# Kernel tuning notes

Measured on AMD Instinct MI355X. Metric: run time of the kernel, lower is better.

## Reference

```python
import jax, jax.numpy as jnp
import numpy as np

B, S, H, NH = 1, 4096, 768, 12
D = H // NH  # per-head dim = 64


def setup_inputs() -> dict:
    key = jax.random.key(0)
    ks = jax.random.split(key, 10)
    p = 0.02  # param scale
    return {
        "x": jax.random.normal(ks[0], (B, S, H), jnp.float32),
        "Wq": jax.random.normal(ks[1], (H, H), jnp.float32) * p,
        "bq": jax.random.normal(ks[2], (H,), jnp.float32) * p,
        "Wk": jax.random.normal(ks[3], (H, H), jnp.float32) * p,
        "bk": jax.random.normal(ks[4], (H,), jnp.float32) * p,
        "Wv": jax.random.normal(ks[5], (H, H), jnp.float32) * p,
        "bv": jax.random.normal(ks[6], (H,), jnp.float32) * p,
        "Wo": jax.random.normal(ks[7], (H, H), jnp.float32) * p,
        "bo": jax.random.normal(ks[8], (H,), jnp.float32) * p,
        "attn_mask": jax.random.randint(ks[9], (B, 1, 1, S), 0, 2).astype(bool),
    }


def _split_heads(t):
    # [B, S, H] -> [B, NH, S, D]
    return t.reshape(B, S, NH, D).transpose(0, 2, 1, 3)


def reference(x, Wq, bq, Wk, bk, Wv, bv, Wo, bo, attn_mask):
    q = _split_heads(x @ Wq.T + bq)
    k = _split_heads(x @ Wk.T + bk)
    v = _split_heads(x @ Wv.T + bv)
    scores = jnp.einsum('bhqd,bhkd->bhqk', q, k) / np.sqrt(D).astype(np.float32)
    scores = jnp.where(attn_mask, jnp.float32(-1e9), scores)
    attn = jax.nn.softmax(scores, axis=-1)
    ctx = jnp.einsum('bhqk,bhkd->bhqd', attn, v)
    ctx = ctx.transpose(0, 2, 1, 3).reshape(B, S, H)  # merge heads
    return ctx @ Wo.T + bo
```

## Files before the change

kernel.cpp:

```cpp
#include <hip/hip_runtime.h>
#include <stdint.h>

#define S_LEN 4096
#define HDIM  768
#define NHEAD 12
#define DHEAD 64

typedef _Float16 f16;
typedef __attribute__((ext_vector_type(8)))  _Float16 f16x8;
typedef __attribute__((ext_vector_type(4)))  _Float16 f16x4;
typedef __attribute__((ext_vector_type(4)))  float    f32x4;
typedef __attribute__((ext_vector_type(16))) float    f32x16;

typedef __attribute__((address_space(1))) void gv_t;
typedef __attribute__((address_space(3))) void lv_t;

__device__ __forceinline__ void async_copy16(const void* g, void* l) {
  __builtin_amdgcn_global_load_lds((gv_t*)g, (lv_t*)l, 16, 0, 0);
}

__device__ __forceinline__ float fast_exp2(float x) {
#if __has_builtin(__builtin_amdgcn_exp2f)
  return __builtin_amdgcn_exp2f(x);
#else
  return exp2f(x);
#endif
}

__device__ __forceinline__ int swz4(int row) { return (row ^ (row >> 2)) & 3; }

constexpr size_t OFF_META = 0;
constexpr size_t OFF_RIDX = 256;
constexpr size_t OFF_XB   = 65536;
constexpr size_t SZ_XB    = (size_t)S_LEN * HDIM * 2;
constexpr size_t OFF_WQKV = OFF_XB + SZ_XB;
constexpr size_t SZ_WQKV  = (size_t)3 * HDIM * HDIM * 2;
constexpr size_t OFF_WO   = OFF_WQKV + SZ_WQKV;
constexpr size_t SZ_WO    = (size_t)HDIM * HDIM * 2;
constexpr size_t OFF_Q    = OFF_WO + SZ_WO;
constexpr size_t SZ_HD    = (size_t)NHEAD * S_LEN * DHEAD * 2;
constexpr size_t OFF_K    = OFF_Q + SZ_HD;
constexpr size_t OFF_VT   = OFF_K + SZ_HD;
constexpr size_t OFF_VR   = OFF_VT + SZ_HD;
constexpr size_t OFF_PO1  = OFF_VR + SZ_HD;

__global__ __launch_bounds__(256) void k_prep(const float* __restrict__ x,
                                              const float* __restrict__ wq,
                                              const float* __restrict__ wk,
                                              const float* __restrict__ wv,
                                              const float* __restrict__ wo,
                                              const int* __restrict__ mi,
                                              f16* __restrict__ dst,
                                              int* __restrict__ ridx,
                                              int* __restrict__ meta) {
  __shared__ int s_flag;
  __shared__ int s_cnt[256];
  const int b = blockIdx.x, tid = threadIdx.x;
  if (b < 5376) {
    int i = b * 256 + tid;
    const float* src; int off;
    if (i < 786432) { src = x; off = i; }
    else {
      int j = i - 786432;
      int w = j / 147456;
      off = j - w * 147456;
      src = (w == 0) ? wq : (w == 1) ? wk : (w == 2) ? wv : wo;
    }
    float4 v = ((const float4*)src)[off];
    f16x4 h;
    h[0] = (f16)v.x; h[1] = (f16)v.y; h[2] = (f16)v.z; h[3] = (f16)v.w;
    ((f16x4*)dst)[i] = h;
    return;
  }
  if (tid == 0) s_flag = 1;
  __syncthreads();
  int bad = 0;
  #pragma unroll
  for (int k = 0; k < 4; ++k) {
    int v = mi[k * 256 + tid];
    if (v != 0 && v != 1) bad = 1;
  }
  if (bad) atomicAnd(&s_flag, 0);
  __syncthreads();
  const int isInt = s_flag;
  const unsigned char* mu8 = (const unsigned char*)mi;
  int keep[16]; int cnt = 0;
  const int s0 = tid * 16;
  #pragma unroll
  for (int k = 0; k < 16; ++k) {
    int mval = isInt ? mi[s0 + k] : (int)mu8[s0 + k];
    keep[k] = (mval == 0) ? 1 : 0;
    cnt += keep[k];
    ridx[s0 + k] = 0;
  }
  s_cnt[tid] = cnt;
  __syncthreads();
  for (int off = 1; off < 256; off <<= 1) {
    int t = (tid >= off) ? s_cnt[tid - off] : 0;
    __syncthreads();
    s_cnt[tid] += t;
    __syncthreads();
  }
  int base = s_cnt[tid] - cnt;
  #pragma unroll
  for (int k = 0; k < 16; ++k) {
    if (keep[k]) { ridx[base] = s0 + k; ++base; }
  }
  if (tid == 255) meta[0] = s_cnt[255];
}

__global__ __launch_bounds__(256) void k_qkv(
    const f16* __restrict__ xb, const f16* __restrict__ wqkv,
    const float* __restrict__ bq, const float* __restrict__ bk, const float* __restrict__ bv,
    const int* __restrict__ ridx, const int* __restrict__ meta,
    f16* __restrict__ Qh, f16* __restrict__ Kc, f16* __restrict__ Vtc) {
  __shared__ __attribute__((aligned(16))) f16 lA[128 * 32];
  __shared__ __attribute__((aligned(16))) f16 lB[128 * 32];
  __shared__ __attribute__((aligned(16))) f16 lT[64 * 132];
  const int tid = threadIdx.x;
  const int wid = tid >> 6, lane = tid & 63;
  const int hf = lane >> 5, l31 = lane & 31;
  const int wm = wid >> 1, wn = wid & 1;
  const int tn = blockIdx.x;
  const int m0 = blockIdx.y * 128;
  const int mat = tn / 6;
  const int nb = (tn % 6) * 128;
  const int kc = meta[0];
  const int kcp = (kc + 63) & ~63;
  if (mat != 0 && m0 >= kc) return;
  const f16* wbase = wqkv + (size_t)mat * HDIM * HDIM;

  const int ar0 = tid >> 2, ar1 = 64 + (tid >> 2);
  const f16* asrc0;
  const f16* asrc1;
  if (mat == 0) {
    asrc0 = xb + (size_t)(m0 + ar0) * HDIM;
    asrc1 = xb + (size_t)(m0 + ar1) * HDIM;
  } else {
    int g0 = (m0 + ar0 < kc) ? ridx[m0 + ar0] : 0;
    int g1 = (m0 + ar1 < kc) ? ridx[m0 + ar1] : 0;
    asrc0 = xb + (size_t)g0 * HDIM;
    asrc1 = xb + (size_t)g1 * HDIM;
  }
  const int slot = tid & 3;
  const int gs0 = slot ^ swz4(ar0);
  const int gs1 = slot ^ swz4(ar1);

  f32x16 acc[2][2] = {};

  for (int k0 = 0; k0 < HDIM; k0 += 32) {
    async_copy16((const char*)(asrc0 + k0) + gs0 * 16, (char*)lA + (wid * 64) * 16);
    async_copy16((const char*)(asrc1 + k0) + gs1 * 16, (char*)lA + (256 + wid * 64) * 16);
    async_copy16((const char*)(wbase + (size_t)(nb + ar0) * HDIM + k0) + gs0 * 16,
                 (char*)lB + (wid * 64) * 16);
    async_copy16((const char*)(wbase + (size_t)(nb + ar1) * HDIM + k0) + gs1 * 16,
                 (char*)lB + (256 + wid * 64) * 16);
    __syncthreads();
    #pragma unroll
    for (int kk = 0; kk < 2; ++kk) {
      f16x8 af[2], bf[2];
      #pragma unroll
      for (int mi = 0; mi < 2; ++mi) {
        int row = wm * 64 + mi * 32 + l31;
        af[mi] = *(const f16x8*)&lA[row * 32 + (((kk * 2 + hf) ^ swz4(row)) * 8)];
      }
      #pragma unroll
      for (int ni = 0; ni < 2; ++ni) {
        int row = wn * 64 + ni * 32 + l31;
        bf[ni] = *(const f16x8*)&lB[row * 32 + (((kk * 2 + hf) ^ swz4(row)) * 8)];
      }
      #pragma unroll
      for (int mi = 0; mi < 2; ++mi)
        #pragma unroll
        for (int ni = 0; ni < 2; ++ni)
          acc[mi][ni] = __builtin_amdgcn_mfma_f32_32x32x16_f16(af[mi], bf[ni], acc[mi][ni], 0, 0, 0);
    }
    __syncthreads();
  }

  if (mat == 2) {
    const float* bias = bv;
    #pragma unroll
    for (int pass = 0; pass < 2; ++pass) {
      __syncthreads();
      if (wn == pass) {
        #pragma unroll
        for (int ni = 0; ni < 2; ++ni) {
          const int n = nb + wn * 64 + ni * 32 + l31;
          const float bn = bias[n];
          const int dloc = ni * 32 + l31;
          #pragma unroll
          for (int mi = 0; mi < 2; ++mi) {
            #pragma unroll
            for (int rg = 0; rg < 4; ++rg) {
              const int sbase = wm * 64 + mi * 32 + 8 * rg + 4 * hf;
              f16x4 v4;
              #pragma unroll
              for (int j = 0; j < 4; ++j) {
                const int s = m0 + sbase + j;
                v4[j] = (s < kc) ? (f16)(acc[mi][ni][rg * 4 + j] + bn) : (f16)0.f;
              }
              *(f16x4*)&lT[dloc * 132 + sbase] = v4;
            }
          }
        }
      }
      __syncthreads();
      const int headg = (nb >> 6) + pass;
      for (int u = tid; u < 1024; u += 256) {
        const int d = u >> 4, p8 = u & 15;
        const int base16 = (p8 >> 1) * 16, half = p8 & 1;
        f16x4 lo = *(const f16x4*)&lT[d * 132 + base16 + half * 4];
        f16x4 hi = *(const f16x4*)&lT[d * 132 + base16 + 8 + half * 4];
        f16x8 o;
        o[0] = lo[0]; o[1] = lo[1]; o[2] = lo[2]; o[3] = lo[3];
        o[4] = hi[0]; o[5] = hi[1]; o[6] = hi[2]; o[7] = hi[3];
        *(f16x8*)&Vtc[((size_t)headg * DHEAD + d) * S_LEN + m0 + p8 * 8] = o;
      }
    }
    return;
  }

  const float* bias = (mat == 0) ? bq : bk;
  const float qscale = 0.125f * 1.44269504088896341f;
  #pragma unroll
  for (int mi = 0; mi < 2; ++mi) {
    #pragma unroll
    for (int ni = 0; ni < 2; ++ni) {
      int n = nb + wn * 64 + ni * 32 + l31;
      int head = n >> 6, d = n & 63;
      float b = bias[n];
      #pragma unroll
      for (int reg = 0; reg < 16; ++reg) {
        int s = m0 + wm * 64 + mi * 32 + (reg & 3) + 8 * (reg >> 2) + 4 * hf;
        float val = acc[mi][ni][reg] + b;
        if (mat == 0) {
          Qh[((size_t)head * S_LEN + s) * DHEAD + d] = (f16)(val * qscale);
        } else if (s < kc) {
          Kc[((size_t)head * S_LEN + s) * DHEAD + d] = (f16)val;
        } else if (s < kcp) {
          Kc[((size_t)head * S_LEN + s) * DHEAD + d] = (f16)0.f;
        }
      }
    }
  }
}

__global__ __launch_bounds__(256, 3) void k_attn(
    const f16* __restrict__ Qh, const f16* __restrict__ Kc, const f16* __restrict__ Vtc,
    const int* __restrict__ meta, f16* __restrict__ PO0, f16* __restrict__ PO1,
    float* __restrict__ PL) {
  __shared__ __attribute__((aligned(16))) f16 lK[2][64 * 64];
  __shared__ __attribute__((aligned(16))) f16 lV[2][64 * 64];
  const int tid = threadIdx.x;
  const int wid = tid >> 6, lane = tid & 63;
  const int hf = lane >> 5, l31 = lane & 31, r7 = l31 & 7;

  const int lid = blockIdx.x;
  const int w = ((lid & 7) * 96) + (lid >> 3);
  const int head = w >> 6;
  const int rem = w & 63;
  const int split = rem >> 5;
  const int q0 = (rem & 31) * 128 + wid * 32;

  const int kc = meta[0];
  const int nkt = (kc + 63) >> 6;
  const int th = nkt >> 1;
  const int t0 = split ? th : 0;
  const int t1 = split ? nkt : th;

  const f16* Qp = Qh + ((size_t)head * S_LEN + q0 + l31) * DHEAD;
  f16x8 qf[4];
  #pragma unroll
  for (int dc = 0; dc < 4; ++dc) qf[dc] = *(const f16x8*)(Qp + dc * 16 + hf * 8);

  f32x16 accO[2] = {};
  float ls0 = 0.f, ls1 = 0.f, ls2 = 0.f, ls3 = 0.f;

  const char* kbase = (const char*)(Kc + (size_t)head * S_LEN * DHEAD);
  const char* vbase = (const char*)(Vtc + (size_t)head * DHEAD * S_LEN);

  const int c0row = tid >> 3,         c0slot = tid & 7;
  const int c1row = (256 + tid) >> 3, c1slot = tid & 7;
  const int gs0 = c0slot ^ (c0row & 7);
  const int gs1 = c1slot ^ (c1row & 7);

  auto stage = [&](int t, int buf) {
    const int j0 = t * 64;
    async_copy16(kbase + (size_t)(j0 + c0row) * 128 + gs0 * 16,
                 (char*)&lK[buf][0] + (wid * 64) * 16);
    async_copy16(vbase + (size_t)c0row * (S_LEN * 2) + (size_t)j0 * 2 + gs0 * 16,
                 (char*)&lV[buf][0] + (wid * 64) * 16);
    async_copy16(kbase + (size_t)(j0 + c1row) * 128 + gs1 * 16,
                 (char*)&lK[buf][0] + (256 + wid * 64) * 16);
    async_copy16(vbase + (size_t)c1row * (S_LEN * 2) + (size_t)j0 * 2 + gs1 * 16,
                 (char*)&lV[buf][0] + (256 + wid * 64) * 16);
  };

  int cur = 0;
  if (t0 < t1) {
    stage(t0, 0);
    __syncthreads();
  }

  for (int t = t0; t < t1; ++t) {
    const bool more = (t + 1 < t1);
    if (more) stage(t + 1, cur ^ 1);

    #pragma unroll
    for (int mh = 0; mh < 2; ++mh) {
      f16x8 af[4];
      const int arow = mh * 32 + l31;
      #pragma unroll
      for (int dc = 0; dc < 4; ++dc)
        af[dc] = *(const f16x8*)&lK[cur][arow * 64 + ((((dc << 1) | hf) ^ r7) * 8)];
      f32x16 s = {};
      #pragma unroll
      for (int dc = 0; dc < 4; ++dc)
        s = __builtin_amdgcn_mfma_f32_32x32x16_f16(af[dc], qf[dc], s, 0, 0, 0);
      #pragma unroll
      for (int u = 0; u < 16; ++u) {
        s[u] = fast_exp2(s[u]);
        if ((u & 3) == 0) ls0 += s[u];
        else if ((u & 3) == 1) ls1 += s[u];
        else if ((u & 3) == 2) ls2 += s[u];
        else ls3 += s[u];
      }
      #pragma unroll
      for (int cc = 0; cc < 2; ++cc) {
        f16x8 pf;
        #pragma unroll
        for (int u = 0; u < 8; ++u) pf[u] = (f16)s[8 * cc + u];
        const int c2 = mh * 2 + cc;
        #pragma unroll
        for (int dh = 0; dh < 2; ++dh) {
          const int vrow = dh * 32 + l31;
          f16x8 vf = *(const f16x8*)&lV[cur][vrow * 64 + ((((c2 << 1) | hf) ^ r7) * 8)];
          accO[dh] = __builtin_amdgcn_mfma_f32_32x32x16_f16(pf, vf, accO[dh], 0, 0, 0);
        }
      }
    }

    if (more) {
      __syncthreads();
      cur ^= 1;
    }
  }

  float lsum = (ls0 + ls1) + (ls2 + ls3);
  lsum += __shfl_xor(lsum, 32);
  if (split == 1) lsum -= (float)(nkt * 64 - kc);
  if (hf == 0)
    PL[((size_t)split * NHEAD + head) * S_LEN + q0 + l31] = lsum;

  __syncthreads();
  f16* ost = (f16*)lK;
  #pragma unroll
  for (int dh = 0; dh < 2; ++dh)
    #pragma unroll
    for (int reg = 0; reg < 16; ++reg) {
      int row = (reg & 3) + 8 * (reg >> 2) + 4 * hf;
      ost[wid * 2048 + row * 64 + dh * 32 + l31] = (f16)accO[dh][reg];
    }
  f16* PO = split ? PO1 : PO0;
  const f16* osrc = ost + wid * 2048;
  #pragma unroll
  for (int p = 0; p < 4; ++p) {
    int row = p * 8 + (lane >> 3), sl = lane & 7;
    f16x8 v = *(const f16x8*)&osrc[row * 64 + sl * 8];
    *(f16x8*)&PO[((size_t)head * S_LEN + q0 + row) * DHEAD + sl * 8] = v;
  }
}

__global__ __launch_bounds__(256) void k_out(
    const f16* __restrict__ PO0, const f16* __restrict__ PO1,
    const float* __restrict__ PL, const f16* __restrict__ wo,
    const float* __restrict__ bo, float* __restrict__ out) {
  __shared__ __attribute__((aligned(16))) f16 lA[128 * 64];
  __shared__ __attribute__((aligned(16))) f16 lB[64 * 64];
  __shared__ float linv[NHEAD * 128];
  const int tid = threadIdx.x;
  const int wid = tid >> 6, lane = tid & 63;
  const int hf = lane >> 5, l31 = lane & 31;
  const int wm = wid >> 1, wn = wid & 1;
  const int lid = blockIdx.x;
  const int w = ((lid & 7) * 48) + (lid >> 3);
  const int nb = (w % 12) * 64;
  const int m0 = (w / 12) * 128;

  for (int i = tid; i < NHEAD * 128; i += 256) {
    int h = i >> 7, r = i & 127;
    float l = PL[(size_t)h * S_LEN + m0 + r] + PL[(size_t)(NHEAD + h) * S_LEN + m0 + r];
    linv[i] = 1.0f / l;
  }
  __syncthreads();

  f32x16 acc[2] = {};

  for (int head = 0; head < NHEAD; ++head) {
    #pragma unroll
    for (int it = 0; it < 4; ++it) {
      int c = it * 256 + tid;
      int row = c >> 3, slot = c & 7;
      int gs = slot ^ (row & 7);
      size_t pi = ((size_t)head * S_LEN + m0 + row) * DHEAD + gs * 8;
      f16x8 a0 = *(const f16x8*)(PO0 + pi);
      f16x8 a1 = *(const f16x8*)(PO1 + pi);
      float il = linv[head * 128 + row];
      f16x8 av;
      #pragma unroll
      for (int u = 0; u < 8; ++u) av[u] = (f16)(((float)a0[u] + (float)a1[u]) * il);
      *(f16x8*)&lA[c * 8] = av;
    }
    #pragma unroll
    for (int it = 0; it < 2; ++it) {
      int c = it * 256 + tid;
      int row = c >> 3, slot = c & 7;
      int gs = slot ^ (row & 7);
      async_copy16((const char*)(wo + (size_t)(nb + row) * HDIM + head * 64) + gs * 16,
                   (char*)lB + (it * 256 + wid * 64) * 16);
    }
    __syncthreads();
    #pragma unroll
    for (int kk = 0; kk < 4; ++kk) {
      f16x8 af[2], bf;
      #pragma unroll
      for (int mi = 0; mi < 2; ++mi) {
        int row = wm * 64 + mi * 32 + l31;
        af[mi] = *(const f16x8*)&lA[row * 64 + ((((kk << 1) | hf) ^ (row & 7)) * 8)];
      }
      int rb = wn * 32 + l31;
      bf = *(const f16x8*)&lB[rb * 64 + ((((kk << 1) | hf) ^ (rb & 7)) * 8)];
      #pragma unroll
      for (int mi = 0; mi < 2; ++mi)
        acc[mi] = __builtin_amdgcn_mfma_f32_32x32x16_f16(af[mi], bf, acc[mi], 0, 0, 0);
    }
    __syncthreads();
  }

  const int n = nb + wn * 32 + l31;
  const float b = bo[n];
  #pragma unroll
  for (int mi = 0; mi < 2; ++mi) {
    #pragma unroll
    for (int reg = 0; reg < 16; ++reg) {
      int s = m0 + wm * 64 + mi * 32 + (reg & 3) + 8 * (reg >> 2) + 4 * hf;
      out[(size_t)s * HDIM + n] = acc[mi][reg] + b;
    }
  }
}

extern "C" void kernel_launch(void* const* d_in, const int* in_sizes, int n_in,
                              void* d_out, int out_size, void* d_ws, size_t ws_size,
                              hipStream_t stream) {
  const float* x  = (const float*)d_in[0];
  const float* Wq = (const float*)d_in[1];
  const float* bq = (const float*)d_in[2];
  const float* Wk = (const float*)d_in[3];
  const float* bk = (const float*)d_in[4];
  const float* Wv = (const float*)d_in[5];
  const float* bv = (const float*)d_in[6];
  const float* Wo = (const float*)d_in[7];
  const float* bo = (const float*)d_in[8];
  const int*   mask = (const int*)d_in[9];
  float* out = (float*)d_out;

  char* ws = (char*)d_ws;
  int* meta  = (int*)(ws + OFF_META);
  int* ridx  = (int*)(ws + OFF_RIDX);
  f16* xb    = (f16*)(ws + OFF_XB);
  f16* wqkv  = (f16*)(ws + OFF_WQKV);
  f16* wob   = (f16*)(ws + OFF_WO);
  f16* Qh    = (f16*)(ws + OFF_Q);
  f16* Kc    = (f16*)(ws + OFF_K);
  f16* Vtc   = (f16*)(ws + OFF_VT);
  f16* PO0   = (f16*)(ws + OFF_VR);
  f16* PO1   = (f16*)(ws + OFF_PO1);
  float* PL  = (float*)(ws + OFF_WQKV);

  k_prep<<<dim3(5377), 256, 0, stream>>>(x, Wq, Wk, Wv, Wo, mask, xb, ridx, meta);
  k_qkv<<<dim3(18, 32), 256, 0, stream>>>(xb, wqkv, bq, bk, bv, ridx, meta, Qh, Kc, Vtc);
  k_attn<<<dim3(768), 256, 0, stream>>>(Qh, Kc, Vtc, meta, PO0, PO1, PL);
  k_out<<<dim3(384), 256, 0, stream>>>(PO0, PO1, PL, wob, bo, out);
}
```

Before: 170.9 us.

## Drop split-K in attention and normalize outputs inside the attention kernel

The attention kernel no longer splits the key range into two halves. Each 128-thread block now handles 64 queries over all key tiles and divides by the softmax sum itself before writing a single normalized f16 output. This removes the second partial-output buffer, the per-row sum buffer, and the combine-and-normalize step in the output projection, which now loads the attention output straight into LDS with async copies. In exchange, each block has half as many waves sharing every staged K/V tile. That doubles per-thread staging work, cuts the total number of resident waves, and lengthens each block's serial key loop, which may hurt latency hiding.

```diff
diff --git a/kernel.cpp b/kernel.cpp
--- a/kernel.cpp
+++ b/kernel.cpp
@@ -41,8 +41,7 @@
 constexpr size_t SZ_HD    = (size_t)NHEAD * S_LEN * DHEAD * 2;
 constexpr size_t OFF_K    = OFF_Q + SZ_HD;
 constexpr size_t OFF_VT   = OFF_K + SZ_HD;
-constexpr size_t OFF_VR   = OFF_VT + SZ_HD;
-constexpr size_t OFF_PO1  = OFF_VR + SZ_HD;
+constexpr size_t OFF_PO   = OFF_VT + SZ_HD;
 
 __global__ __launch_bounds__(256) void k_prep(const float* __restrict__ x,
                                               const float* __restrict__ wq,
@@ -246,12 +245,12 @@
   }
 }
 
-__global__ __launch_bounds__(256, 3) void k_attn(
+__global__ __launch_bounds__(128, 2) void k_attn(
     const f16* __restrict__ Qh, const f16* __restrict__ Kc, const f16* __restrict__ Vtc,
-    const int* __restrict__ meta, f16* __restrict__ PO0, f16* __restrict__ PO1,
-    float* __restrict__ PL) {
+    const int* __restrict__ meta, f16* __restrict__ PO) {
   __shared__ __attribute__((aligned(16))) f16 lK[2][64 * 64];
   __shared__ __attribute__((aligned(16))) f16 lV[2][64 * 64];
+  __shared__ float lil[64];
   const int tid = threadIdx.x;
   const int wid = tid >> 6, lane = tid & 63;
   const int hf = lane >> 5, l31 = lane & 31, r7 = l31 & 7;
@@ -259,15 +258,10 @@
   const int lid = blockIdx.x;
   const int w = ((lid & 7) * 96) + (lid >> 3);
   const int head = w >> 6;
-  const int rem = w & 63;
-  const int split = rem >> 5;
-  const int q0 = (rem & 31) * 128 + wid * 32;
+  const int q0 = (w & 63) * 64 + wid * 32;
 
   const int kc = meta[0];
   const int nkt = (kc + 63) >> 6;
-  const int th = nkt >> 1;
-  const int t0 = split ? th : 0;
-  const int t1 = split ? nkt : th;
 
   const f16* Qp = Qh + ((size_t)head * S_LEN + q0 + l31) * DHEAD;
   f16x8 qf[4];
@@ -280,31 +274,27 @@
   const char* kbase = (const char*)(Kc + (size_t)head * S_LEN * DHEAD);
   const char* vbase = (const char*)(Vtc + (size_t)head * DHEAD * S_LEN);
 
-  const int c0row = tid >> 3,         c0slot = tid & 7;
-  const int c1row = (256 + tid) >> 3, c1slot = tid & 7;
-  const int gs0 = c0slot ^ (c0row & 7);
-  const int gs1 = c1slot ^ (c1row & 7);
+  const int crow = tid >> 3, cslot = tid & 7;
+  const int gsc = cslot ^ (crow & 7);
 
   auto stage = [&](int t, int buf) {
     const int j0 = t * 64;
-    async_copy16(kbase + (size_t)(j0 + c0row) * 128 + gs0 * 16,
-                 (char*)&lK[buf][0] + (wid * 64) * 16);
-    async_copy16(vbase + (size_t)c0row * (S_LEN * 2) + (size_t)j0 * 2 + gs0 * 16,
-                 (char*)&lV[buf][0] + (wid * 64) * 16);
-    async_copy16(kbase + (size_t)(j0 + c1row) * 128 + gs1 * 16,
-                 (char*)&lK[buf][0] + (256 + wid * 64) * 16);
-    async_copy16(vbase + (size_t)c1row * (S_LEN * 2) + (size_t)j0 * 2 + gs1 * 16,
-                 (char*)&lV[buf][0] + (256 + wid * 64) * 16);
+    #pragma unroll
+    for (int it = 0; it < 4; ++it) {
+      const int row = it * 16 + crow;
+      async_copy16(kbase + (size_t)(j0 + row) * 128 + gsc * 16,
+                   (char*)&lK[buf][0] + (it * 128 + wid * 64) * 16);
+      async_copy16(vbase + (size_t)row * (S_LEN * 2) + (size_t)j0 * 2 + gsc * 16,
+                   (char*)&lV[buf][0] + (it * 128 + wid * 64) * 16);
+    }
   };
 
   int cur = 0;
-  if (t0 < t1) {
-    stage(t0, 0);
-    __syncthreads();
-  }
-
-  for (int t = t0; t < t1; ++t) {
-    const bool more = (t + 1 < t1);
+  stage(0, 0);
+  __syncthreads();
+
+  for (int t = 0; t < nkt; ++t) {
+    const bool more = (t + 1 < nkt);
     if (more) stage(t + 1, cur ^ 1);
 
     #pragma unroll
@@ -349,36 +339,31 @@
 
   float lsum = (ls0 + ls1) + (ls2 + ls3);
   lsum += __shfl_xor(lsum, 32);
-  if (split == 1) lsum -= (float)(nkt * 64 - kc);
-  if (hf == 0)
-    PL[((size_t)split * NHEAD + head) * S_LEN + q0 + l31] = lsum;
-
+  lsum -= (float)(nkt * 64 - kc);
+  if (hf == 0) lil[wid * 32 + l31] = 1.0f / lsum;
   __syncthreads();
-  f16* ost = (f16*)lK;
+
+  f16* ost = (f16*)lK + wid * 2048;
   #pragma unroll
   for (int dh = 0; dh < 2; ++dh)
     #pragma unroll
     for (int reg = 0; reg < 16; ++reg) {
       int row = (reg & 3) + 8 * (reg >> 2) + 4 * hf;
-      ost[wid * 2048 + row * 64 + dh * 32 + l31] = (f16)accO[dh][reg];
-    }
-  f16* PO = split ? PO1 : PO0;
-  const f16* osrc = ost + wid * 2048;
+      ost[row * 64 + dh * 32 + l31] = (f16)(accO[dh][reg] * lil[wid * 32 + row]);
+    }
   #pragma unroll
   for (int p = 0; p < 4; ++p) {
     int row = p * 8 + (lane >> 3), sl = lane & 7;
-    f16x8 v = *(const f16x8*)&osrc[row * 64 + sl * 8];
+    f16x8 v = *(const f16x8*)&ost[row * 64 + sl * 8];
     *(f16x8*)&PO[((size_t)head * S_LEN + q0 + row) * DHEAD + sl * 8] = v;
   }
 }
 
 __global__ __launch_bounds__(256) void k_out(
-    const f16* __restrict__ PO0, const f16* __restrict__ PO1,
-    const float* __restrict__ PL, const f16* __restrict__ wo,
+    const f16* __restrict__ PO, const f16* __restrict__ wo,
     const float* __restrict__ bo, float* __restrict__ out) {
   __shared__ __attribute__((aligned(16))) f16 lA[128 * 64];
   __shared__ __attribute__((aligned(16))) f16 lB[64 * 64];
-  __shared__ float linv[NHEAD * 128];
   const int tid = threadIdx.x;
   const int wid = tid >> 6, lane = tid & 63;
   const int hf = lane >> 5, l31 = lane & 31;
@@ -388,13 +373,6 @@
   const int nb = (w % 12) * 64;
   const int m0 = (w / 12) * 128;
 
-  for (int i = tid; i < NHEAD * 128; i += 256) {
-    int h = i >> 7, r = i & 127;
-    float l = PL[(size_t)h * S_LEN + m0 + r] + PL[(size_t)(NHEAD + h) * S_LEN + m0 + r];
-    linv[i] = 1.0f / l;
-  }
-  __syncthreads();
-
   f32x16 acc[2] = {};
 
   for (int head = 0; head < NHEAD; ++head) {
@@ -403,14 +381,8 @@
       int c = it * 256 + tid;
       int row = c >> 3, slot = c & 7;
       int gs = slot ^ (row & 7);
-      size_t pi = ((size_t)head * S_LEN + m0 + row) * DHEAD + gs * 8;
-      f16x8 a0 = *(const f16x8*)(PO0 + pi);
-      f16x8 a1 = *(const f16x8*)(PO1 + pi);
-      float il = linv[head * 128 + row];
-      f16x8 av;
-      #pragma unroll
-      for (int u = 0; u < 8; ++u) av[u] = (f16)(((float)a0[u] + (float)a1[u]) * il);
-      *(f16x8*)&lA[c * 8] = av;
+      async_copy16((const char*)(PO + ((size_t)head * S_LEN + m0 + row) * DHEAD) + gs * 16,
+                   (char*)lA + (it * 256 + wid * 64) * 16);
     }
     #pragma unroll
     for (int it = 0; it < 2; ++it) {
@@ -474,12 +446,10 @@
   f16* Qh    = (f16*)(ws + OFF_Q);
   f16* Kc    = (f16*)(ws + OFF_K);
   f16* Vtc   = (f16*)(ws + OFF_VT);
-  f16* PO0   = (f16*)(ws + OFF_VR);
-  f16* PO1   = (f16*)(ws + OFF_PO1);
-  float* PL  = (float*)(ws + OFF_WQKV);
+  f16* PO    = (f16*)(ws + OFF_PO);
 
   k_prep<<<dim3(5377), 256, 0, stream>>>(x, Wq, Wk, Wv, Wo, mask, xb, ridx, meta);
   k_qkv<<<dim3(18, 32), 256, 0, stream>>>(xb, wqkv, bq, bk, bv, ridx, meta, Qh, Kc, Vtc);
-  k_attn<<<dim3(768), 256, 0, stream>>>(Qh, Kc, Vtc, meta, PO0, PO1, PL);
-  k_out<<<dim3(384), 256, 0, stream>>>(PO0, PO1, PL, wob, bo, out);
-}
+  k_attn<<<dim3(768), 128, 0, stream>>>(Qh, Kc, Vtc, meta, PO);
+  k_out<<<dim3(384), 256, 0, stream>>>(PO, wob, bo, out);
+}
```

After: 169.0 us. Within noise of the previous version (-1.1%).
